# Optimization experiments

Measured on AMD Instinct MI355X. Metric: run time of the kernel, lower is better.

The kernel has to match this reference:

```python
import jax, jax.numpy as jnp
import numpy as np

B, N, D, H = 4, 4096, 256, 8
HD = D // H
EPS = 1e-09


def _feature_map(t):
    # ELU(x) + 1, strictly positive feature map (Katharopoulos et al. 2020)
    return jax.nn.elu(t) + 1.0


def setup_inputs() -> dict:
    key = jax.random.key(0)
    ks = jax.random.split(key, 8)
    s = 0.02  # weight init scale for numerical stability
    return {
        "x": jax.random.normal(ks[0], (B, N, D), dtype=jnp.float32),
        "prior": jax.random.normal(ks[1], (B, N, N), dtype=jnp.float32),
        "Wq": jax.random.normal(ks[2], (D, D), dtype=jnp.float32) * s,
        "Wk": jax.random.normal(ks[3], (D, D), dtype=jnp.float32) * s,
        "Wv": jax.random.normal(ks[4], (D, D), dtype=jnp.float32) * s,
        "bv": jax.random.normal(ks[5], (D,), dtype=jnp.float32) * s,
        "Wo": jax.random.normal(ks[6], (D, D), dtype=jnp.float32) * s,
        "bo": jax.random.normal(ks[7], (D,), dtype=jnp.float32) * s,
    }


def reference(x, prior, Wq, Wk, Wv, bv, Wo, bo):
    b, n, d = x.shape
    # bias: mean over last axis of prior -> (b, n, 1, 1), broadcast over heads/dims
    bias = jnp.mean(prior, axis=-1)[:, :, None, None]
    q = _feature_map(jnp.einsum("bnd,ed->bne", x, Wq).reshape(b, n, H, HD) + bias)
    padding_mask = jnp.all(q == 0, axis=-1)  # (b, n, H)
    k = _feature_map(jnp.einsum("bnd,ed->bne", x, Wk).reshape(b, n, H, HD))
    v = _feature_map((jnp.einsum("bnd,ed->bne", x, Wv) + bv).reshape(b, n, H, HD))
    # KV summary state: (b, h, m, d) with m = value dim, d = key feature dim
    kv = jnp.einsum("bnhd,bnhm->bhmd", k, v)
    # normalizer: q . sum_n(k)
    z = 1.0 / (jnp.einsum("bnhd,bhd->bnh", q, jnp.sum(k, axis=1)) + EPS)
    attn = jnp.einsum("bnhd,bhmd,bnh->bnhm", q, kv, z)
    attn = jnp.where(padding_mask[..., None], 0.0, attn)
    attn = attn.reshape(b, n, H * HD)
    return jnp.einsum("bnd,ed->bne", attn, Wo) + bo
```

## Files before the change

kernel.cpp:

```cpp
#include <hip/hip_runtime.h>
#include <hip/hip_bf16.h>
#include <math.h>

#define B_ 4
#define N_ 4096
#define D_ 256
#define H_ 8
#define HD_ 32
#define TOKENS (B_ * N_)
#define EPSF 1e-9f
#define KV_CH 64

typedef __bf16 bf16x8 __attribute__((ext_vector_type(8)));
typedef float f32x4 __attribute__((ext_vector_type(4)));
typedef ushort ushort8_t __attribute__((ext_vector_type(8)));

__device__ __forceinline__ float elu1(float x) { return x > 0.f ? x + 1.f : __expf(x); }

__device__ __forceinline__ ushort f2bf(float f) {
    __hip_bfloat16 h = __float2bfloat16(f);
    return *reinterpret_cast<ushort*>(&h);
}

#define GLOAD_LDS16(g, l)                                                              \
    __builtin_amdgcn_global_load_lds((__attribute__((address_space(1))) const void*)(g), \
                                     (__attribute__((address_space(3))) void*)(l), 16, 0, 0)

#define MFMA16(a, b, c) __builtin_amdgcn_mfma_f32_16x16x32_bf16((a), (b), (c), 0, 0, 0)

__global__ __launch_bounds__(256) void k_cvt_w(const float* __restrict__ Wq,
                                               const float* __restrict__ Wk,
                                               const float* __restrict__ Wv,
                                               const float* __restrict__ Wo,
                                               ushort* __restrict__ dst) {
    const int i = blockIdx.x * 256 + threadIdx.x;
    const int sel = i >> 13;
    const float* src = sel == 0 ? Wq : sel == 1 ? Wk : sel == 2 ? Wv : Wo;
    const int j = i & 8191;
    const float4* s = (const float4*)src + (size_t)j * 2;
    const float4 a = s[0], b = s[1];
    ushort8_t o;
    o[0] = f2bf(a.x); o[1] = f2bf(a.y); o[2] = f2bf(a.z); o[3] = f2bf(a.w);
    o[4] = f2bf(b.x); o[5] = f2bf(b.y); o[6] = f2bf(b.z); o[7] = f2bf(b.w);
    *((ushort8_t*)dst + i) = o;
}

__global__ __launch_bounds__(512, 2) void k_mix2(const float* __restrict__ prior,
                                                 const float* __restrict__ x,
                                                 const ushort* __restrict__ wq,
                                                 const ushort* __restrict__ wk,
                                                 const ushort* __restrict__ wv,
                                                 const float* __restrict__ bv,
                                                 float* __restrict__ bias_g,
                                                 ushort* __restrict__ qpre,
                                                 ushort* __restrict__ kb,
                                                 ushort* __restrict__ vb) {
    __shared__ ushort As[32 * 256];
    __shared__ ushort Ws[3 * 256 * 32];
    const int t = threadIdx.x;
    const int w = t >> 6, lane = t & 63;
    const int bid = blockIdx.x;

    if (bid % 5 != 0) {
        const int bidx = bid - bid / 5 - 1;
        const int row = bidx * 8 + w;
        const f32x4* p = (const f32x4*)(prior + (size_t)row * N_);
        float s0 = 0.f, s1 = 0.f, s2 = 0.f, s3 = 0.f;
#pragma unroll
        for (int i = 0; i < 4; ++i) {
            const f32x4 a = __builtin_nontemporal_load(p + (i * 4 + 0) * 64 + lane);
            const f32x4 b = __builtin_nontemporal_load(p + (i * 4 + 1) * 64 + lane);
            const f32x4 c = __builtin_nontemporal_load(p + (i * 4 + 2) * 64 + lane);
            const f32x4 d = __builtin_nontemporal_load(p + (i * 4 + 3) * 64 + lane);
            s0 += a[0] + a[1] + a[2] + a[3];
            s1 += b[0] + b[1] + b[2] + b[3];
            s2 += c[0] + c[1] + c[2] + c[3];
            s3 += d[0] + d[1] + d[2] + d[3];
        }
        float s = (s0 + s1) + (s2 + s3);
#pragma unroll
        for (int off = 32; off; off >>= 1) s += __shfl_xor(s, off, 64);
        if (lane == 0) bias_g[row] = s * (1.0f / N_);
        return;
    }

    const int rowBase = (bid / 5) * 32;

    {
        const int r = t >> 4;
        const int c0 = (t & 15) * 4;
#pragma unroll
        for (int j = 0; j < 4; ++j) {
            const int c = c0 + j * 64;
            const float4 xv = *(const float4*)(x + (size_t)(rowBase + r) * 256 + c);
            ushort4 o;
            o.x = f2bf(xv.x); o.y = f2bf(xv.y); o.z = f2bf(xv.z); o.w = f2bf(xv.w);
            const int byte = (r * 512 + c * 2) ^ ((r & 7) << 4);
            *(ushort4*)((char*)As + byte) = o;
        }
    }

    const int wr = w >> 2, wc = w & 3;
    const int q_ = lane >> 4;
    f32x4 accq[4] = {}, acck[4] = {}, accv[4] = {};

    for (int kt = 0; kt < 256; kt += 32) {
        __syncthreads();
#pragma unroll
        for (int j = 0; j < 6; ++j) {
            const int c = j * 512 + t;
            const int idx = c & 1023;
            const int e = idx >> 2;
            const int pslot = idx & 3;
            const int qsrc = pslot ^ ((e >> 1) & 3);
            const ushort* srcm = (j < 2) ? wq : (j < 4) ? wk : wv;
            GLOAD_LDS16(srcm + (size_t)e * 256 + kt + qsrc * 8, (char*)Ws + c * 16);
        }
        __syncthreads();
        const int r = wr * 16 + (lane & 15);
        const int abyte = (r * 512 + (kt + q_ * 8) * 2) ^ ((r & 7) << 4);
        const bf16x8 af = *(const bf16x8*)((const char*)As + abyte);
#pragma unroll
        for (int n = 0; n < 4; ++n) {
            const int e = wc * 64 + n * 16 + (lane & 15);
            const int wbyte = e * 64 + ((q_ ^ ((e >> 1) & 3)) * 16);
            const bf16x8 bq = *(const bf16x8*)((const char*)Ws + wbyte);
            const bf16x8 bk = *(const bf16x8*)((const char*)Ws + 16384 + wbyte);
            const bf16x8 bw = *(const bf16x8*)((const char*)Ws + 32768 + wbyte);
            accq[n] = MFMA16(af, bq, accq[n]);
            acck[n] = MFMA16(af, bk, acck[n]);
            accv[n] = MFMA16(af, bw, accv[n]);
        }
    }

#pragma unroll
    for (int n = 0; n < 4; ++n)
#pragma unroll
        for (int j = 0; j < 4; ++j) {
            const int rl = wr * 16 + (lane >> 4) * 4 + j;
            const int col = wc * 64 + n * 16 + (lane & 15);
            const size_t go = (size_t)(rowBase + rl) * 256 + col;
            qpre[go] = f2bf(accq[n][j]);
            kb[go]   = f2bf(elu1(acck[n][j]));
            vb[go]   = f2bf(elu1(accv[n][j] + bv[col]));
        }
}

__global__ __launch_bounds__(256) void k_kvpart(const ushort* __restrict__ kmat,
                                                const ushort* __restrict__ vmat,
                                                float* __restrict__ part) {
    const int bh = blockIdx.x;
    const int b = bh >> 3, h = bh & 7;
    const int tok0 = b * N_ + blockIdx.y * 64;
    __shared__ float kt_[64][32];
    __shared__ float vt_[64][32];
    const int t = threadIdx.x;
    const int m = t >> 3;
    const int lvec = (t & 7) * 4;
#pragma unroll
    for (int half = 0; half < 2; ++half) {
        const int rr = (t >> 3) + half * 32;
        const size_t g = (size_t)(tok0 + rr) * D_ + h * HD_ + lvec;
        const ushort4 ku = *(const ushort4*)(kmat + g);
        const ushort4 vu = *(const ushort4*)(vmat + g);
        kt_[rr][lvec + 0] = __bfloat162float(*(const __hip_bfloat16*)&ku.x);
        kt_[rr][lvec + 1] = __bfloat162float(*(const __hip_bfloat16*)&ku.y);
        kt_[rr][lvec + 2] = __bfloat162float(*(const __hip_bfloat16*)&ku.z);
        kt_[rr][lvec + 3] = __bfloat162float(*(const __hip_bfloat16*)&ku.w);
        vt_[rr][lvec + 0] = __bfloat162float(*(const __hip_bfloat16*)&vu.x);
        vt_[rr][lvec + 1] = __bfloat162float(*(const __hip_bfloat16*)&vu.y);
        vt_[rr][lvec + 2] = __bfloat162float(*(const __hip_bfloat16*)&vu.z);
        vt_[rr][lvec + 3] = __bfloat162float(*(const __hip_bfloat16*)&vu.w);
    }
    __syncthreads();
    float4 acc = {0.f, 0.f, 0.f, 0.f};
    float4 sk = {0.f, 0.f, 0.f, 0.f};
#pragma unroll 4
    for (int r = 0; r < 64; ++r) {
        const float vv = vt_[r][m];
        const float4 kk = *(const float4*)&kt_[r][lvec];
        acc.x = fmaf(vv, kk.x, acc.x);
        acc.y = fmaf(vv, kk.y, acc.y);
        acc.z = fmaf(vv, kk.z, acc.z);
        acc.w = fmaf(vv, kk.w, acc.w);
        sk.x += kk.x; sk.y += kk.y; sk.z += kk.z; sk.w += kk.w;
    }
    float* outp = part + ((size_t)blockIdx.y * 32 + bh) * 1056;
    *(float4*)(outp + m * 32 + lvec) = acc;
    if (m == 0) *(float4*)(outp + 1024 + lvec) = sk;
}

__global__ __launch_bounds__(256) void k_kvred(const float* __restrict__ part,
                                               float* __restrict__ kv,
                                               float* __restrict__ ksum) {
    const int i = blockIdx.x * 256 + threadIdx.x;
    if (i >= 32 * 1056) return;
    const int bh = i / 1056, r = i - bh * 1056;
    float s = 0.f;
#pragma unroll 8
    for (int c = 0; c < KV_CH; ++c) s += part[((size_t)c * 32 + bh) * 1056 + r];
    if (r < 1024) kv[(size_t)bh * 1024 + r] = s;
    else          ksum[(size_t)bh * 32 + (r - 1024)] = s;
}

__global__ __launch_bounds__(512, 2) void k_fusedB(const ushort* __restrict__ qpre,
                                                   const float* __restrict__ bias_g,
                                                   const float* __restrict__ kv,
                                                   const float* __restrict__ ksum,
                                                   const ushort* __restrict__ wo,
                                                   const float* __restrict__ bo,
                                                   float* __restrict__ out) {
    __shared__ ushort qs[64 * 256];
    __shared__ ushort at_s[64 * 256];
    __shared__ ushort Ws2[256 * 32];
    const int t = threadIdx.x;
    const int w = t >> 6, lane = t & 63;
    const int tokBase = blockIdx.x * 64;
    const int b = tokBase >> 12;

#pragma unroll
    for (int j = 0; j < 4; ++j) {
        const int chunk = j * 512 + t;
        GLOAD_LDS16(qpre + (size_t)tokBase * 256 + (size_t)chunk * 8,
                    (char*)qs + chunk * 16);
    }

    const int c = t & 255;
    const int h = c >> 5, m = c & 31;
    f32x4 kvr[8], ksr[8];
#pragma unroll
    for (int i = 0; i < 8; ++i) {
        kvr[i] = *(const f32x4*)(kv + (((size_t)(b * H_ + h) * HD_ + m) * HD_) + i * 4);
        ksr[i] = *(const f32x4*)(ksum + (size_t)(b * H_ + h) * HD_ + i * 4);
    }
    __syncthreads();

    {
        const int r = t >> 3;
        const float brow = bias_g[tokBase + r];
        const int cb = (t & 7) * 32;
#pragma unroll
        for (int i = 0; i < 4; ++i) {
            bf16x8 qv = *(bf16x8*)(qs + r * 256 + cb + i * 8);
#pragma unroll
            for (int j = 0; j < 8; ++j) qv[j] = (__bf16)elu1((float)qv[j] + brow);
            *(bf16x8*)(qs + r * 256 + cb + i * 8) = qv;
        }
    }
    __syncthreads();

    for (int tok2 = 0; tok2 < 32; ++tok2) {
        const int tok = tok2 * 2 + (t >> 8);
        float num = 0.f, den = 0.f;
#pragma unroll
        for (int i = 0; i < 4; ++i) {
            const bf16x8 qv = *(const bf16x8*)(qs + tok * 256 + h * HD_ + i * 8);
#pragma unroll
            for (int j = 0; j < 8; ++j) {
                const float qf = (float)qv[j];
                num = fmaf(qf, ((const float*)kvr)[i * 8 + j], num);
                den = fmaf(qf, ((const float*)ksr)[i * 8 + j], den);
            }
        }
        const float a = num / (den + EPSF);
        const int byte = (tok * 512 + c * 2) ^ ((tok & 7) << 4);
        *(ushort*)((char*)at_s + byte) = f2bf(a);
    }

    const int wr = w >> 2, wc = w & 3;
    const int q_ = lane >> 4;
    f32x4 acc[2][4] = {};
    for (int kt = 0; kt < 256; kt += 32) {
        __syncthreads();
#pragma unroll
        for (int j = 0; j < 2; ++j) {
            const int ch = j * 512 + t;
            const int e = ch >> 2;
            const int pslot = ch & 3;
            const int qsrc = pslot ^ ((e >> 1) & 3);
            GLOAD_LDS16(wo + (size_t)e * 256 + kt + qsrc * 8, (char*)Ws2 + ch * 16);
        }
        __syncthreads();
        bf16x8 af[2];
#pragma unroll
        for (int mm = 0; mm < 2; ++mm) {
            const int r = wr * 32 + mm * 16 + (lane & 15);
            const int byte = (r * 512 + (kt + q_ * 8) * 2) ^ ((r & 7) << 4);
            af[mm] = *(const bf16x8*)((const char*)at_s + byte);
        }
#pragma unroll
        for (int n = 0; n < 4; ++n) {
            const int e = wc * 64 + n * 16 + (lane & 15);
            const int wbyte = e * 64 + ((q_ ^ ((e >> 1) & 3)) * 16);
            const bf16x8 bw = *(const bf16x8*)((const char*)Ws2 + wbyte);
#pragma unroll
            for (int mm = 0; mm < 2; ++mm)
                acc[mm][n] = MFMA16(af[mm], bw, acc[mm][n]);
        }
    }
#pragma unroll
    for (int mm = 0; mm < 2; ++mm)
#pragma unroll
        for (int n = 0; n < 4; ++n)
#pragma unroll
            for (int j = 0; j < 4; ++j) {
                const int row = tokBase + wr * 32 + mm * 16 + (lane >> 4) * 4 + j;
                const int col = wc * 64 + n * 16 + (lane & 15);
                out[(size_t)row * 256 + col] = acc[mm][n][j] + bo[col];
            }
}

extern "C" void kernel_launch(void* const* d_in, const int* in_sizes, int n_in,
                              void* d_out, int out_size, void* d_ws, size_t ws_size,
                              hipStream_t stream) {
    const float* x     = (const float*)d_in[0];
    const float* prior = (const float*)d_in[1];
    const float* Wq    = (const float*)d_in[2];
    const float* Wk    = (const float*)d_in[3];
    const float* Wv    = (const float*)d_in[4];
    const float* bv    = (const float*)d_in[5];
    const float* Wo    = (const float*)d_in[6];
    const float* bo    = (const float*)d_in[7];
    float* out = (float*)d_out;

    char* w8 = (char*)d_ws;
    ushort* qpre = (ushort*)w8;
    ushort* kb   = qpre + (size_t)TOKENS * D_;
    ushort* vb   = kb + (size_t)TOKENS * D_;
    ushort* wqb  = vb + (size_t)TOKENS * D_;
    ushort* wkb  = wqb + 65536;
    ushort* wvb  = wkb + 65536;
    ushort* wob  = wvb + 65536;
    float* kvb   = (float*)(wqb + 4 * 65536);
    float* ksb   = kvb + 32768;
    float* bias  = ksb + 1024;
    float* part  = bias + TOKENS;

    k_cvt_w<<<128, 256, 0, stream>>>(Wq, Wk, Wv, Wo, wqb);

    k_mix2<<<2560, 512, 0, stream>>>(prior, x, wqb, wkb, wvb, bv, bias, qpre, kb, vb);

    k_kvpart<<<dim3(32, KV_CH), 256, 0, stream>>>(kb, vb, part);
    k_kvred<<<132, 256, 0, stream>>>(part, kvb, ksb);

    k_fusedB<<<256, 512, 0, stream>>>(qpre, bias, kvb, ksb, wob, bo, out);
}
```

Baseline: 103.3 us.

## Retile QKV projection into 128x128 GEMM tiles with pre-converted bf16 x

Adds a separate kernel that converts x to bf16 ahead of time. The fused QKV projection is rewritten as a 128x128-tile GEMM over the concatenated Wq/Wk/Wv weights, where each block produces one output slice. The prior-mean reduction blocks are interleaved 8:3 with the GEMM blocks, and each reduction block now handles two rows per wave. This gives more MFMA reuse per LDS load than the old 32-row tile that re-streamed all three weight matrices. The cost is an extra launch and an extra round trip of x through memory.

```diff
diff --git a/kernel.cpp b/kernel.cpp
--- a/kernel.cpp
+++ b/kernel.cpp
@@ -45,105 +45,111 @@
     *((ushort8_t*)dst + i) = o;
 }
 
-__global__ __launch_bounds__(512, 2) void k_mix2(const float* __restrict__ prior,
-                                                 const float* __restrict__ x,
-                                                 const ushort* __restrict__ wq,
-                                                 const ushort* __restrict__ wk,
-                                                 const ushort* __restrict__ wv,
-                                                 const float* __restrict__ bv,
-                                                 float* __restrict__ bias_g,
-                                                 ushort* __restrict__ qpre,
-                                                 ushort* __restrict__ kb,
-                                                 ushort* __restrict__ vb) {
-    __shared__ ushort As[32 * 256];
-    __shared__ ushort Ws[3 * 256 * 32];
+__global__ __launch_bounds__(256) void k_cvt(const float* __restrict__ src,
+                                             ushort* __restrict__ dst) {
+    const int i = blockIdx.x * 256 + threadIdx.x;
+    const float4* s = (const float4*)src + (size_t)i * 2;
+    const float4 a = s[0], b = s[1];
+    ushort8_t o;
+    o[0] = f2bf(a.x); o[1] = f2bf(a.y); o[2] = f2bf(a.z); o[3] = f2bf(a.w);
+    o[4] = f2bf(b.x); o[5] = f2bf(b.y); o[6] = f2bf(b.z); o[7] = f2bf(b.w);
+    *((ushort8_t*)dst + i) = o;
+}
+
+__global__ __launch_bounds__(256) void k_mix5(const float* __restrict__ prior,
+                                              const ushort* __restrict__ xb,
+                                              const ushort* __restrict__ wall,
+                                              const float* __restrict__ bv,
+                                              float* __restrict__ bias_g,
+                                              ushort* __restrict__ qpre,
+                                              ushort* __restrict__ kb,
+                                              ushort* __restrict__ vb) {
+    __shared__ ushort As[128 * 32];
+    __shared__ ushort Bs[128 * 32];
     const int t = threadIdx.x;
     const int w = t >> 6, lane = t & 63;
     const int bid = blockIdx.x;
-
-    if (bid % 5 != 0) {
-        const int bidx = bid - bid / 5 - 1;
-        const int row = bidx * 8 + w;
-        const f32x4* p = (const f32x4*)(prior + (size_t)row * N_);
-        float s0 = 0.f, s1 = 0.f, s2 = 0.f, s3 = 0.f;
-#pragma unroll
-        for (int i = 0; i < 4; ++i) {
-            const f32x4 a = __builtin_nontemporal_load(p + (i * 4 + 0) * 64 + lane);
-            const f32x4 b = __builtin_nontemporal_load(p + (i * 4 + 1) * 64 + lane);
-            const f32x4 c = __builtin_nontemporal_load(p + (i * 4 + 2) * 64 + lane);
-            const f32x4 d = __builtin_nontemporal_load(p + (i * 4 + 3) * 64 + lane);
-            s0 += a[0] + a[1] + a[2] + a[3];
-            s1 += b[0] + b[1] + b[2] + b[3];
-            s2 += c[0] + c[1] + c[2] + c[3];
-            s3 += d[0] + d[1] + d[2] + d[3];
-        }
-        float s = (s0 + s1) + (s2 + s3);
-#pragma unroll
-        for (int off = 32; off; off >>= 1) s += __shfl_xor(s, off, 64);
-        if (lane == 0) bias_g[row] = s * (1.0f / N_);
+    const int grp = bid / 11, pos = bid % 11;
+
+    if (pos >= 3) {
+        const int base = (grp * 8 + (pos - 3)) * 8;
+#pragma unroll
+        for (int rr = 0; rr < 2; ++rr) {
+            const int row = base + w + rr * 4;
+            const f32x4* p = (const f32x4*)(prior + (size_t)row * N_);
+            float s0 = 0.f, s1 = 0.f, s2 = 0.f, s3 = 0.f;
+#pragma unroll
+            for (int i = 0; i < 4; ++i) {
+                const f32x4 a = __builtin_nontemporal_load(p + (i * 4 + 0) * 64 + lane);
+                const f32x4 b = __builtin_nontemporal_load(p + (i * 4 + 1) * 64 + lane);
+                const f32x4 c = __builtin_nontemporal_load(p + (i * 4 + 2) * 64 + lane);
+                const f32x4 d = __builtin_nontemporal_load(p + (i * 4 + 3) * 64 + lane);
+                s0 += a[0] + a[1] + a[2] + a[3];
+                s1 += b[0] + b[1] + b[2] + b[3];
+                s2 += c[0] + c[1] + c[2] + c[3];
+                s3 += d[0] + d[1] + d[2] + d[3];
+            }
+            float s = (s0 + s1) + (s2 + s3);
+#pragma unroll
+            for (int off = 32; off; off >>= 1) s += __shfl_xor(s, off, 64);
+            if (lane == 0) bias_g[row] = s * (1.0f / N_);
+        }
         return;
     }
 
-    const int rowBase = (bid / 5) * 32;
-
-    {
-        const int r = t >> 4;
-        const int c0 = (t & 15) * 4;
-#pragma unroll
-        for (int j = 0; j < 4; ++j) {
-            const int c = c0 + j * 64;
-            const float4 xv = *(const float4*)(x + (size_t)(rowBase + r) * 256 + c);
-            ushort4 o;
-            o.x = f2bf(xv.x); o.y = f2bf(xv.y); o.z = f2bf(xv.z); o.w = f2bf(xv.w);
-            const int byte = (r * 512 + c * 2) ^ ((r & 7) << 4);
-            *(ushort4*)((char*)As + byte) = o;
-        }
-    }
-
-    const int wr = w >> 2, wc = w & 3;
-    const int q_ = lane >> 4;
-    f32x4 accq[4] = {}, acck[4] = {}, accv[4] = {};
-
+    const int qi = grp * 3 + pos;
+    const int bx = qi & 127, by = qi >> 7;
+    const int rowBase = bx * 128;
+    const int eBase = by * 128;
+    const int sel = eBase >> 8;
+    const int colOff = eBase & 255;
+    const int wr = w >> 1, wc = w & 1;
+    const int srow = lane >> 2;
+    const int scol = (lane & 3) * 8;
+
+    f32x4 acc[4][4] = {};
     for (int kt = 0; kt < 256; kt += 32) {
         __syncthreads();
 #pragma unroll
-        for (int j = 0; j < 6; ++j) {
-            const int c = j * 512 + t;
-            const int idx = c & 1023;
-            const int e = idx >> 2;
-            const int pslot = idx & 3;
-            const int qsrc = pslot ^ ((e >> 1) & 3);
-            const ushort* srcm = (j < 2) ? wq : (j < 4) ? wk : wv;
-            GLOAD_LDS16(srcm + (size_t)e * 256 + kt + qsrc * 8, (char*)Ws + c * 16);
+        for (int c = 0; c < 2; ++c) {
+            const int chunk = w * 2 + c;
+            const int r = chunk * 16 + srow;
+            GLOAD_LDS16(xb + (size_t)(rowBase + r) * 256 + kt + scol, As + chunk * 512);
+            GLOAD_LDS16(wall + (size_t)(eBase + r) * 256 + kt + scol, Bs + chunk * 512);
         }
         __syncthreads();
-        const int r = wr * 16 + (lane & 15);
-        const int abyte = (r * 512 + (kt + q_ * 8) * 2) ^ ((r & 7) << 4);
-        const bf16x8 af = *(const bf16x8*)((const char*)As + abyte);
+        bf16x8 af[4], bfr[4];
+#pragma unroll
+        for (int m = 0; m < 4; ++m) {
+            const int r = wr * 64 + m * 16 + (lane & 15);
+            af[m] = *reinterpret_cast<const bf16x8*>(&As[r * 32 + (lane >> 4) * 8]);
+        }
 #pragma unroll
         for (int n = 0; n < 4; ++n) {
-            const int e = wc * 64 + n * 16 + (lane & 15);
-            const int wbyte = e * 64 + ((q_ ^ ((e >> 1) & 3)) * 16);
-            const bf16x8 bq = *(const bf16x8*)((const char*)Ws + wbyte);
-            const bf16x8 bk = *(const bf16x8*)((const char*)Ws + 16384 + wbyte);
-            const bf16x8 bw = *(const bf16x8*)((const char*)Ws + 32768 + wbyte);
-            accq[n] = MFMA16(af, bq, accq[n]);
-            acck[n] = MFMA16(af, bk, acck[n]);
-            accv[n] = MFMA16(af, bw, accv[n]);
-        }
-    }
-
-#pragma unroll
-    for (int n = 0; n < 4; ++n)
-#pragma unroll
-        for (int j = 0; j < 4; ++j) {
-            const int rl = wr * 16 + (lane >> 4) * 4 + j;
-            const int col = wc * 64 + n * 16 + (lane & 15);
-            const size_t go = (size_t)(rowBase + rl) * 256 + col;
-            qpre[go] = f2bf(accq[n][j]);
-            kb[go]   = f2bf(elu1(acck[n][j]));
-            vb[go]   = f2bf(elu1(accv[n][j] + bv[col]));
-        }
+            const int c2 = wc * 64 + n * 16 + (lane & 15);
+            bfr[n] = *reinterpret_cast<const bf16x8*>(&Bs[c2 * 32 + (lane >> 4) * 8]);
+        }
+#pragma unroll
+        for (int m = 0; m < 4; ++m)
+#pragma unroll
+            for (int n = 0; n < 4; ++n)
+                acc[m][n] = MFMA16(af[m], bfr[n], acc[m][n]);
+    }
+
+#pragma unroll
+    for (int m = 0; m < 4; ++m)
+#pragma unroll
+        for (int n = 0; n < 4; ++n)
+#pragma unroll
+            for (int j = 0; j < 4; ++j) {
+                const int row = rowBase + wr * 64 + m * 16 + (lane >> 4) * 4 + j;
+                const int col = colOff + wc * 64 + n * 16 + (lane & 15);
+                const size_t go = (size_t)row * 256 + col;
+                const float v = acc[m][n][j];
+                if (sel == 0)      qpre[go] = f2bf(v);
+                else if (sel == 1) kb[go]   = f2bf(elu1(v));
+                else               vb[go]   = f2bf(elu1(v + bv[col]));
+            }
 }
 
 __global__ __launch_bounds__(256) void k_kvpart(const ushort* __restrict__ kmat,
@@ -327,18 +333,18 @@
     ushort* qpre = (ushort*)w8;
     ushort* kb   = qpre + (size_t)TOKENS * D_;
     ushort* vb   = kb + (size_t)TOKENS * D_;
-    ushort* wqb  = vb + (size_t)TOKENS * D_;
-    ushort* wkb  = wqb + 65536;
-    ushort* wvb  = wkb + 65536;
-    ushort* wob  = wvb + 65536;
+    ushort* xb   = vb + (size_t)TOKENS * D_;
+    ushort* wqb  = xb + (size_t)TOKENS * D_;
+    ushort* wob  = wqb + 3 * 65536;
     float* kvb   = (float*)(wqb + 4 * 65536);
     float* ksb   = kvb + 32768;
     float* bias  = ksb + 1024;
     float* part  = bias + TOKENS;
 
     k_cvt_w<<<128, 256, 0, stream>>>(Wq, Wk, Wv, Wo, wqb);
-
-    k_mix2<<<2560, 512, 0, stream>>>(prior, x, wqb, wkb, wvb, bv, bias, qpre, kb, vb);
+    k_cvt<<<2048, 256, 0, stream>>>(x, xb);
+
+    k_mix5<<<2816, 256, 0, stream>>>(prior, xb, wqb, bv, bias, qpre, kb, vb);
 
     k_kvpart<<<dim3(32, KV_CH), 256, 0, stream>>>(kb, vb, part);
     k_kvred<<<132, 256, 0, stream>>>(part, kvb, ksb);
```

Result: slower. 119.4 us (+15.6%).

## Interleave prior row-mean reduction into QKV projection k-loop instead of separate blocks

Applied to the files above, without the earlier changes.

Previously the fused launch split blocks between prior-mean reduction (4 of every 5 blocks) and QKV GEMM (1 of 5). Now each GEMM block also streams its 32 rows of prior, spreading the loads across the 8 k-tile iterations so the memory traffic overlaps the MFMA work. The grid drops from 2560 to 512 blocks. This risks lower memory-level parallelism and higher register pressure in the GEMM loop.

```diff
diff --git a/kernel.cpp b/kernel.cpp
--- a/kernel.cpp
+++ b/kernel.cpp
@@ -45,7 +45,7 @@
     *((ushort8_t*)dst + i) = o;
 }
 
-__global__ __launch_bounds__(512, 2) void k_mix2(const float* __restrict__ prior,
+__global__ __launch_bounds__(512, 2) void k_mix6(const float* __restrict__ prior,
                                                  const float* __restrict__ x,
                                                  const ushort* __restrict__ wq,
                                                  const ushort* __restrict__ wk,
@@ -60,31 +60,7 @@
     const int t = threadIdx.x;
     const int w = t >> 6, lane = t & 63;
     const int bid = blockIdx.x;
-
-    if (bid % 5 != 0) {
-        const int bidx = bid - bid / 5 - 1;
-        const int row = bidx * 8 + w;
-        const f32x4* p = (const f32x4*)(prior + (size_t)row * N_);
-        float s0 = 0.f, s1 = 0.f, s2 = 0.f, s3 = 0.f;
-#pragma unroll
-        for (int i = 0; i < 4; ++i) {
-            const f32x4 a = __builtin_nontemporal_load(p + (i * 4 + 0) * 64 + lane);
-            const f32x4 b = __builtin_nontemporal_load(p + (i * 4 + 1) * 64 + lane);
-            const f32x4 c = __builtin_nontemporal_load(p + (i * 4 + 2) * 64 + lane);
-            const f32x4 d = __builtin_nontemporal_load(p + (i * 4 + 3) * 64 + lane);
-            s0 += a[0] + a[1] + a[2] + a[3];
-            s1 += b[0] + b[1] + b[2] + b[3];
-            s2 += c[0] + c[1] + c[2] + c[3];
-            s3 += d[0] + d[1] + d[2] + d[3];
-        }
-        float s = (s0 + s1) + (s2 + s3);
-#pragma unroll
-        for (int off = 32; off; off >>= 1) s += __shfl_xor(s, off, 64);
-        if (lane == 0) bias_g[row] = s * (1.0f / N_);
-        return;
-    }
-
-    const int rowBase = (bid / 5) * 32;
+    const int rowBase = bid * 32;
 
     {
         const int r = t >> 4;
@@ -100,11 +76,17 @@
         }
     }
 
+    const int brow0 = rowBase + w * 4;
+    const f32x4* bp = (const f32x4*)(prior + (size_t)brow0 * N_);
+    float s0 = 0.f, s1 = 0.f, s2 = 0.f, s3 = 0.f;
+
     const int wr = w >> 2, wc = w & 3;
     const int q_ = lane >> 4;
     f32x4 accq[4] = {}, acck[4] = {}, accv[4] = {};
 
-    for (int kt = 0; kt < 256; kt += 32) {
+#pragma unroll
+    for (int it = 0; it < 8; ++it) {
+        const int kt = it * 32;
         __syncthreads();
 #pragma unroll
         for (int j = 0; j < 6; ++j) {
@@ -115,6 +97,20 @@
             const int qsrc = pslot ^ ((e >> 1) & 3);
             const ushort* srcm = (j < 2) ? wq : (j < 4) ? wk : wv;
             GLOAD_LDS16(srcm + (size_t)e * 256 + kt + qsrc * 8, (char*)Ws + c * 16);
+        }
+        {
+            const int br = it >> 1, half = it & 1;
+            const f32x4* rp = bp + (size_t)br * 1024 + half * 512 + lane;
+            float ps = 0.f;
+#pragma unroll
+            for (int i = 0; i < 8; ++i) {
+                const f32x4 v = __builtin_nontemporal_load(rp + i * 64);
+                ps += (v[0] + v[1]) + (v[2] + v[3]);
+            }
+            if (br == 0) s0 += ps;
+            else if (br == 1) s1 += ps;
+            else if (br == 2) s2 += ps;
+            else s3 += ps;
         }
         __syncthreads();
         const int r = wr * 16 + (lane & 15);
@@ -132,6 +128,15 @@
             accv[n] = MFMA16(af, bw, accv[n]);
         }
     }
+
+#define BIAS_RED(sv, rr)                                                    \
+    {                                                                       \
+        float v_ = sv;                                                      \
+        for (int off = 32; off; off >>= 1) v_ += __shfl_xor(v_, off, 64);   \
+        if (lane == 0) bias_g[brow0 + rr] = v_ * (1.0f / N_);               \
+    }
+    BIAS_RED(s0, 0) BIAS_RED(s1, 1) BIAS_RED(s2, 2) BIAS_RED(s3, 3)
+#undef BIAS_RED
 
 #pragma unroll
     for (int n = 0; n < 4; ++n)
@@ -318,8 +323,8 @@
     const float* Wq    = (const float*)d_in[2];
     const float* Wk    = (const float*)d_in[3];
     const float* Wv    = (const float*)d_in[4];
+    const float* Wo    = (const float*)d_in[5 + 1];
     const float* bv    = (const float*)d_in[5];
-    const float* Wo    = (const float*)d_in[6];
     const float* bo    = (const float*)d_in[7];
     float* out = (float*)d_out;
 
@@ -338,7 +343,7 @@
 
     k_cvt_w<<<128, 256, 0, stream>>>(Wq, Wk, Wv, Wo, wqb);
 
-    k_mix2<<<2560, 512, 0, stream>>>(prior, x, wqb, wkb, wvb, bv, bias, qpre, kb, vb);
+    k_mix6<<<512, 512, 0, stream>>>(prior, x, wqb, wkb, wvb, bv, bias, qpre, kb, vb);
 
     k_kvpart<<<dim3(32, KV_CH), 256, 0, stream>>>(kb, vb, part);
     k_kvred<<<132, 256, 0, stream>>>(part, kvb, ksb);
```

After: 136.0 us. 1.32x slower.

## Split QKV projection blocks per matrix and rebalance prior-mean blocks

Applied to the files above, without the earlier changes.

The fused projection kernel now gives each of Q, K and V its own 256-thread block (32 rows by 256 columns) instead of one 512-thread block computing all three. It uses a 7-block group pattern: 3 GEMM blocks plus 4 prior-row-mean blocks, each handling 8 rows. Shared memory per block drops to a single weight tile and launch bounds move to 256 threads with 4 blocks per CU, aiming for higher occupancy and finer-grained scheduling alongside the bandwidth-bound prior reduction. The trade-off is that the x tile is loaded and converted to bf16 three times, once per matrix, and each GEMM block now covers 32 rows per warp.

```diff
diff --git a/kernel.cpp b/kernel.cpp
--- a/kernel.cpp
+++ b/kernel.cpp
@@ -45,7 +45,7 @@
     *((ushort8_t*)dst + i) = o;
 }
 
-__global__ __launch_bounds__(512, 2) void k_mix2(const float* __restrict__ prior,
+__global__ __launch_bounds__(256, 4) void k_mix7(const float* __restrict__ prior,
                                                  const float* __restrict__ x,
                                                  const ushort* __restrict__ wq,
                                                  const ushort* __restrict__ wk,
@@ -56,42 +56,47 @@
                                                  ushort* __restrict__ kb,
                                                  ushort* __restrict__ vb) {
     __shared__ ushort As[32 * 256];
-    __shared__ ushort Ws[3 * 256 * 32];
+    __shared__ ushort Ws[256 * 32];
     const int t = threadIdx.x;
     const int w = t >> 6, lane = t & 63;
     const int bid = blockIdx.x;
-
-    if (bid % 5 != 0) {
-        const int bidx = bid - bid / 5 - 1;
-        const int row = bidx * 8 + w;
-        const f32x4* p = (const f32x4*)(prior + (size_t)row * N_);
-        float s0 = 0.f, s1 = 0.f, s2 = 0.f, s3 = 0.f;
-#pragma unroll
-        for (int i = 0; i < 4; ++i) {
-            const f32x4 a = __builtin_nontemporal_load(p + (i * 4 + 0) * 64 + lane);
-            const f32x4 b = __builtin_nontemporal_load(p + (i * 4 + 1) * 64 + lane);
-            const f32x4 c = __builtin_nontemporal_load(p + (i * 4 + 2) * 64 + lane);
-            const f32x4 d = __builtin_nontemporal_load(p + (i * 4 + 3) * 64 + lane);
-            s0 += a[0] + a[1] + a[2] + a[3];
-            s1 += b[0] + b[1] + b[2] + b[3];
-            s2 += c[0] + c[1] + c[2] + c[3];
-            s3 += d[0] + d[1] + d[2] + d[3];
-        }
-        float s = (s0 + s1) + (s2 + s3);
-#pragma unroll
-        for (int off = 32; off; off >>= 1) s += __shfl_xor(s, off, 64);
-        if (lane == 0) bias_g[row] = s * (1.0f / N_);
+    const int grp = bid / 7, pos = bid % 7;
+
+    if (pos >= 3) {
+        const int base = (grp * 4 + (pos - 3)) * 8;
+#pragma unroll
+        for (int rr = 0; rr < 2; ++rr) {
+            const int row = base + w + rr * 4;
+            const f32x4* p = (const f32x4*)(prior + (size_t)row * N_);
+            float s0 = 0.f, s1 = 0.f, s2 = 0.f, s3 = 0.f;
+#pragma unroll
+            for (int i = 0; i < 4; ++i) {
+                const f32x4 a = __builtin_nontemporal_load(p + (i * 4 + 0) * 64 + lane);
+                const f32x4 b = __builtin_nontemporal_load(p + (i * 4 + 1) * 64 + lane);
+                const f32x4 c = __builtin_nontemporal_load(p + (i * 4 + 2) * 64 + lane);
+                const f32x4 d = __builtin_nontemporal_load(p + (i * 4 + 3) * 64 + lane);
+                s0 += a[0] + a[1] + a[2] + a[3];
+                s1 += b[0] + b[1] + b[2] + b[3];
+                s2 += c[0] + c[1] + c[2] + c[3];
+                s3 += d[0] + d[1] + d[2] + d[3];
+            }
+            float s = (s0 + s1) + (s2 + s3);
+#pragma unroll
+            for (int off = 32; off; off >>= 1) s += __shfl_xor(s, off, 64);
+            if (lane == 0) bias_g[row] = s * (1.0f / N_);
+        }
         return;
     }
 
-    const int rowBase = (bid / 5) * 32;
+    const ushort* wm = pos == 0 ? wq : pos == 1 ? wk : wv;
+    const int rowBase = grp * 32;
 
     {
-        const int r = t >> 4;
-        const int c0 = (t & 15) * 4;
-#pragma unroll
-        for (int j = 0; j < 4; ++j) {
-            const int c = c0 + j * 64;
+        const int r = t >> 3;
+        const int c0 = (t & 7) * 4;
+#pragma unroll
+        for (int j = 0; j < 8; ++j) {
+            const int c = c0 + j * 32;
             const float4 xv = *(const float4*)(x + (size_t)(rowBase + r) * 256 + c);
             ushort4 o;
             o.x = f2bf(xv.x); o.y = f2bf(xv.y); o.z = f2bf(xv.z); o.w = f2bf(xv.w);
@@ -100,50 +105,52 @@
         }
     }
 
-    const int wr = w >> 2, wc = w & 3;
     const int q_ = lane >> 4;
-    f32x4 accq[4] = {}, acck[4] = {}, accv[4] = {};
+    f32x4 acc[2][4] = {};
 
     for (int kt = 0; kt < 256; kt += 32) {
         __syncthreads();
 #pragma unroll
-        for (int j = 0; j < 6; ++j) {
-            const int c = j * 512 + t;
-            const int idx = c & 1023;
-            const int e = idx >> 2;
-            const int pslot = idx & 3;
+        for (int j = 0; j < 4; ++j) {
+            const int cc = j * 256 + t;
+            const int e = cc >> 2;
+            const int pslot = cc & 3;
             const int qsrc = pslot ^ ((e >> 1) & 3);
-            const ushort* srcm = (j < 2) ? wq : (j < 4) ? wk : wv;
-            GLOAD_LDS16(srcm + (size_t)e * 256 + kt + qsrc * 8, (char*)Ws + c * 16);
+            GLOAD_LDS16(wm + (size_t)e * 256 + kt + qsrc * 8, (char*)Ws + cc * 16);
         }
         __syncthreads();
-        const int r = wr * 16 + (lane & 15);
-        const int abyte = (r * 512 + (kt + q_ * 8) * 2) ^ ((r & 7) << 4);
-        const bf16x8 af = *(const bf16x8*)((const char*)As + abyte);
+        bf16x8 af[2];
+#pragma unroll
+        for (int m = 0; m < 2; ++m) {
+            const int r = m * 16 + (lane & 15);
+            const int abyte = (r * 512 + (kt + q_ * 8) * 2) ^ ((r & 7) << 4);
+            af[m] = *(const bf16x8*)((const char*)As + abyte);
+        }
 #pragma unroll
         for (int n = 0; n < 4; ++n) {
-            const int e = wc * 64 + n * 16 + (lane & 15);
+            const int e = w * 64 + n * 16 + (lane & 15);
             const int wbyte = e * 64 + ((q_ ^ ((e >> 1) & 3)) * 16);
-            const bf16x8 bq = *(const bf16x8*)((const char*)Ws + wbyte);
-            const bf16x8 bk = *(const bf16x8*)((const char*)Ws + 16384 + wbyte);
-            const bf16x8 bw = *(const bf16x8*)((const char*)Ws + 32768 + wbyte);
-            accq[n] = MFMA16(af, bq, accq[n]);
-            acck[n] = MFMA16(af, bk, acck[n]);
-            accv[n] = MFMA16(af, bw, accv[n]);
-        }
-    }
-
-#pragma unroll
-    for (int n = 0; n < 4; ++n)
-#pragma unroll
-        for (int j = 0; j < 4; ++j) {
-            const int rl = wr * 16 + (lane >> 4) * 4 + j;
-            const int col = wc * 64 + n * 16 + (lane & 15);
-            const size_t go = (size_t)(rowBase + rl) * 256 + col;
-            qpre[go] = f2bf(accq[n][j]);
-            kb[go]   = f2bf(elu1(acck[n][j]));
-            vb[go]   = f2bf(elu1(accv[n][j] + bv[col]));
-        }
+            const bf16x8 bw = *(const bf16x8*)((const char*)Ws + wbyte);
+#pragma unroll
+            for (int m = 0; m < 2; ++m)
+                acc[m][n] = MFMA16(af[m], bw, acc[m][n]);
+        }
+    }
+
+#pragma unroll
+    for (int m = 0; m < 2; ++m)
+#pragma unroll
+        for (int n = 0; n < 4; ++n)
+#pragma unroll
+            for (int j = 0; j < 4; ++j) {
+                const int rl = m * 16 + (lane >> 4) * 4 + j;
+                const int col = w * 64 + n * 16 + (lane & 15);
+                const size_t go = (size_t)(rowBase + rl) * 256 + col;
+                const float v = acc[m][n][j];
+                if (pos == 0)      qpre[go] = f2bf(v);
+                else if (pos == 1) kb[go]   = f2bf(elu1(v));
+                else               vb[go]   = f2bf(elu1(v + bv[col]));
+            }
 }
 
 __global__ __launch_bounds__(256) void k_kvpart(const ushort* __restrict__ kmat,
@@ -338,7 +345,7 @@
 
     k_cvt_w<<<128, 256, 0, stream>>>(Wq, Wk, Wv, Wo, wqb);
 
-    k_mix2<<<2560, 512, 0, stream>>>(prior, x, wqb, wkb, wvb, bv, bias, qpre, kb, vb);
+    k_mix7<<<3584, 256, 0, stream>>>(prior, x, wqb, wkb, wvb, bv, bias, qpre, kb, vb);
 
     k_kvpart<<<dim3(32, KV_CH), 256, 0, stream>>>(kb, vb, part);
     k_kvred<<<132, 256, 0, stream>>>(part, kvb, ksb);
```

After: 113.5 us. 9.8% more time.
